# Performance work log

Measured on AMD Instinct MI355X. Metric: run time of the kernel, lower is better.

## Reference

```python
import jax, jax.numpy as jnp
import numpy as np

T, D_MODEL, D_FF, N_EXPERTS, TOP_K = 8192, 1024, 4096, 8, 2

def setup_inputs() -> dict:
    key = jax.random.key(0)
    k1, k2, k3, k4, k5 = jax.random.split(key, 5)
    hidden_states = jax.random.normal(k1, (T, D_MODEL), dtype=jnp.float32)
    # router picks TOP_K distinct-ish experts per token; build one-hot mask [T, K, E]
    expert_idx = jax.random.randint(k2, (T, TOP_K), 0, N_EXPERTS)
    selected_experts = jax.nn.one_hot(expert_idx, N_EXPERTS, dtype=jnp.int32)
    rw = jax.random.uniform(k3, (T, TOP_K), dtype=jnp.float32)
    routing_weights = rw / jnp.sum(rw, axis=-1, keepdims=True)
    scale = 1.0 / np.sqrt(D_MODEL)
    wi = jax.random.normal(k4, (N_EXPERTS, D_FF, D_MODEL), dtype=jnp.float32) * scale
    wo = jax.random.normal(k5, (N_EXPERTS, D_MODEL, D_FF), dtype=jnp.float32) * (1.0 / np.sqrt(D_FF))
    return {"hidden_states": hidden_states, "selected_experts": selected_experts,
            "routing_weights": routing_weights, "wi": wi, "wo": wo}

def reference(hidden_states, selected_experts, routing_weights, wi, wo):
    # expert_mask: [E, K, T] (as in torch permute(2,1,0))
    mask = jnp.transpose(selected_experts, (2, 1, 0)).astype(hidden_states.dtype)
    # combined per-token weight for each expert: w[t, e] = sum_k mask[e,k,t]*routing_weights[t,k]
    w = jnp.einsum('ekt,tk->te', mask, routing_weights)
    out = jnp.zeros_like(hidden_states)
    # fixed small loop over experts; tokens not routed to expert e get weight 0,
    # so this is mathematically identical to the gather->MLP->scale->scatter-add.
    for e in range(wi.shape[0]):
        h = jax.nn.relu(hidden_states @ wi[e].T)     # [T, d_ff] (dropout is identity at eval)
        y = h @ wo[e].T                              # [T, d_model]
        out = out + w[:, e:e + 1] * y
    return out
```

## Files before the change

kernel.cpp:

```cpp
#include <hip/hip_runtime.h>
#include <hip/hip_bf16.h>


#define T_TOK   8192
#define D_MODEL 1024
#define D_FF    4096
#define NE      8
#define BM      128
#define BK      64
#define MT2     72
#define MT_MAX  (MT2 * 2)
#define ROWS_MAX (MT2 * 256)
#define BUFB    32768
#define LDS_G1  98304

typedef float f32x4 __attribute__((ext_vector_type(4)));
typedef short s16x8 __attribute__((ext_vector_type(8)));
typedef short s16x4 __attribute__((ext_vector_type(4)));
typedef unsigned short u16;

__device__ __forceinline__ u16 f2bf(float x) {
  __hip_bfloat16 h = __float2bfloat16(x);
  return *reinterpret_cast<u16*>(&h);
}

__device__ __forceinline__ s16x8 cvt8(float4 a, float4 b) {
  s16x8 v;
  v[0] = (short)f2bf(a.x); v[1] = (short)f2bf(a.y);
  v[2] = (short)f2bf(a.z); v[3] = (short)f2bf(a.w);
  v[4] = (short)f2bf(b.x); v[5] = (short)f2bf(b.y);
  v[6] = (short)f2bf(b.z); v[7] = (short)f2bf(b.w);
  return v;
}

__device__ __forceinline__ void gload_lds16(const void* g, void* l) {
  __builtin_amdgcn_global_load_lds((const __attribute__((address_space(1))) void*)g,
                                   (__attribute__((address_space(3))) void*)l,
                                   16, 0, 0);
}

__global__ void moe_route(const int* __restrict__ sel, const float* __restrict__ rw,
                          int* __restrict__ cnt, int* __restrict__ tidx,
                          float* __restrict__ tw) {
  int t = blockIdx.x * blockDim.x + threadIdx.x;
  if (t >= T_TOK) return;
  int e0 = 0, e1 = 0;
  #pragma unroll
  for (int e = 0; e < NE; ++e) {
    if (sel[t * 16 + e])     e0 = e;
    if (sel[t * 16 + 8 + e]) e1 = e;
  }
  float w0 = rw[2 * t], w1 = rw[2 * t + 1];
  if (e0 == e1) {
    int p = atomicAdd(&cnt[e0], 1);
    tidx[e0 * T_TOK + p] = t; tw[e0 * T_TOK + p] = w0 + w1;
  } else {
    int p = atomicAdd(&cnt[e0], 1);
    tidx[e0 * T_TOK + p] = t; tw[e0 * T_TOK + p] = w0;
    int q = atomicAdd(&cnt[e1], 1);
    tidx[e1 * T_TOK + q] = t; tw[e1 * T_TOK + q] = w1;
  }
}

__global__ void moe_tilemap(const int* __restrict__ cnt, const int* __restrict__ tidx,
                            const float* __restrict__ tw, int* __restrict__ te128,
                            int* __restrict__ te256, int* __restrict__ tokr,
                            float* __restrict__ wr) {
  int off[NE + 1];
  {
    int o = 0;
    #pragma unroll
    for (int e = 0; e < NE; ++e) { off[e] = o; o += (cnt[e] + 255) & ~255; }
    off[NE] = o;
  }
  const int total = off[NE];
  const int gid = blockIdx.x * blockDim.x + threadIdx.x;
  const int stride = gridDim.x * blockDim.x;
  for (int t = gid; t < MT_MAX; t += stride) {
    int r0 = t * 128; int e = -1;
    if (r0 < total) {
      #pragma unroll
      for (int i = NE - 1; i >= 0; --i) if (r0 >= off[i]) { e = i; break; }
    }
    te128[t] = e;
    if ((t & 1) == 0) te256[t >> 1] = e;
  }
  for (int i = gid; i < ROWS_MAX; i += stride) {
    if (i >= total) { tokr[i] = -1; wr[i] = 0.f; continue; }
    int e = 0;
    #pragma unroll
    for (int k = NE - 1; k >= 0; --k) if (i >= off[k]) { e = k; break; }
    int j = i - off[e];
    int ok = j < cnt[e];
    tokr[i] = ok ? tidx[e * T_TOK + j] : -1;
    wr[i]   = ok ? tw[e * T_TOK + j] : 0.f;
  }
}

__global__ void moe_gather_x(const float* __restrict__ hs, const int* __restrict__ tokr,
                             u16* __restrict__ Xg) {
  int row = blockIdx.x;
  int tok = tokr[row];
  int c = threadIdx.x * 4;
  u16* dst = Xg + (size_t)row * D_MODEL + c;
  s16x4 o;
  if (tok < 0) {
    o[0] = o[1] = o[2] = o[3] = 0;
  } else {
    float4 v = *(const float4*)(hs + (size_t)tok * D_MODEL + c);
    o[0] = (short)f2bf(v.x); o[1] = (short)f2bf(v.y);
    o[2] = (short)f2bf(v.z); o[3] = (short)f2bf(v.w);
  }
  *(s16x4*)dst = o;
}

__global__ void moe_cvt_w(const float* __restrict__ wi, const float* __restrict__ wo,
                          u16* __restrict__ wib, u16* __restrict__ wob) {
  const size_t NW = (size_t)NE * D_FF * D_MODEL;
  size_t i = ((size_t)blockIdx.x * blockDim.x + threadIdx.x) * 8;
  const float* src; u16* dst;
  if (i < NW) { src = wi + i; dst = wib + i; }
  else        { src = wo + (i - NW); dst = wob + (i - NW); }
  float4 a = *(const float4*)(src);
  float4 b = *(const float4*)(src + 4);
  *(s16x8*)dst = cvt8(a, b);
}

__global__ void moe_cvt_wi_s(const float* __restrict__ wi, u16* __restrict__ wis,
                             int W, int f0) {
  size_t i = ((size_t)blockIdx.x * blockDim.x + threadIdx.x) * 8;
  size_t per = (size_t)W * D_MODEL;
  int e = (int)(i / per); size_t r = i % per;
  const float* src = wi + ((size_t)e * D_FF + f0) * D_MODEL + r;
  float4 a = *(const float4*)src;
  float4 b = *(const float4*)(src + 4);
  *(s16x8*)(wis + i) = cvt8(a, b);
}

__global__ void moe_cvt_wo_s(const float* __restrict__ wo, u16* __restrict__ wos,
                             int W, int f0) {
  size_t i = ((size_t)blockIdx.x * blockDim.x + threadIdx.x) * 8;
  size_t per = (size_t)D_MODEL * W;
  int e = (int)(i / per); size_t r = i % per;
  int row = (int)(r / W), col = (int)(r % W);
  const float* src = wo + ((size_t)e * D_MODEL + row) * D_FF + f0 + col;
  float4 a = *(const float4*)src;
  float4 b = *(const float4*)(src + 4);
  *(s16x8*)(wos + i) = cvt8(a, b);
}

template <bool FULL>
__global__ __launch_bounds__(512, 1)
void moe_g1(const u16* __restrict__ Xg, const u16* __restrict__ wiP,
            const int* __restrict__ te256, u16* __restrict__ H,
            int W, int f0) {
  extern __shared__ char lds[];
  const int GR = gridDim.x;
  const int task = (blockIdx.x & 7) * (GR >> 3) + (blockIdx.x >> 3);
  const int mt = task % MT2;
  const int nc = task / MT2;
  const int e = te256[mt];
  if (e < 0) return;
  const int grow0 = mt * 256;
  const int fcol = nc * 256;

  const int tid = threadIdx.x;
  const int lane = tid & 63, wv = tid >> 6;
  const int lg = lane >> 4, ll = lane & 15;
  const int wm = wv >> 2, wn = wv & 3;

  const int sw = (tid * 16) ^ (((tid >> 3) & 7) << 4);
  const int srow = sw >> 6, scol = sw & 63;
  const int inner = (ll * 64 + lg * 16) ^ (((ll >> 1) & 7) << 4);

  const char* gA = (const char*)(Xg + (size_t)grow0 * D_MODEL);
  const char* gB = (const char*)(wiP + (FULL ? ((size_t)e * D_FF + f0 + fcol)
                                             : ((size_t)e * W + fcol)) * D_MODEL);

  f32x4 acc[8][4];
  #pragma unroll
  for (int m = 0; m < 8; ++m)
    #pragma unroll
    for (int n = 0; n < 4; ++n) acc[m][n] = (f32x4){0.f, 0.f, 0.f, 0.f};

  auto stage = [&](int kb, char* lbuf) {
    #pragma unroll
    for (int j = 0; j < 2; ++j)
      gload_lds16(gA + (size_t)(j * 128 + srow) * 2048 + kb + scol,
                  lbuf + j * 8192 + tid * 16);
    #pragma unroll
    for (int j = 0; j < 2; ++j)
      gload_lds16(gB + (size_t)(j * 128 + srow) * 2048 + kb + scol,
                  lbuf + 16384 + j * 8192 + tid * 16);
  };

  const int NT = D_MODEL / 32;
  stage(0, lds);
  stage(64, lds + BUFB);
  int bufi = 0;
  for (int t = 0; t < NT; ++t) {
    if (t < NT - 1) { asm volatile("s_waitcnt vmcnt(4)" ::: "memory"); }
    else            { asm volatile("s_waitcnt vmcnt(0)" ::: "memory"); }
    asm volatile("s_barrier" ::: "memory");
    const char* la = lds + bufi * BUFB + wm * 8192;
    const char* lb = lds + bufi * BUFB + 16384 + wn * 4096;
    if (t + 2 < NT) {
      int b2 = bufi + 2; if (b2 >= 3) b2 -= 3;
      stage((t + 2) * 64, lds + b2 * BUFB);
    }
    s16x8 bq0 = *(const s16x8*)(lb + 0 * 1024 + inner);
    s16x8 bq1 = *(const s16x8*)(lb + 1 * 1024 + inner);
    s16x8 bq2 = *(const s16x8*)(lb + 2 * 1024 + inner);
    s16x8 bq3 = *(const s16x8*)(lb + 3 * 1024 + inner);
    {
      s16x8 a0 = *(const s16x8*)(la + 0 * 1024 + inner);
      s16x8 a1 = *(const s16x8*)(la + 1 * 1024 + inner);
      s16x8 a2 = *(const s16x8*)(la + 2 * 1024 + inner);
      s16x8 a3 = *(const s16x8*)(la + 3 * 1024 + inner);
      __builtin_amdgcn_s_setprio(1);
      acc[0][0] = __builtin_amdgcn_mfma_f32_16x16x32_bf16(a0, bq0, acc[0][0], 0, 0, 0);
      acc[0][1] = __builtin_amdgcn_mfma_f32_16x16x32_bf16(a0, bq1, acc[0][1], 0, 0, 0);
      acc[0][2] = __builtin_amdgcn_mfma_f32_16x16x32_bf16(a0, bq2, acc[0][2], 0, 0, 0);
      acc[0][3] = __builtin_amdgcn_mfma_f32_16x16x32_bf16(a0, bq3, acc[0][3], 0, 0, 0);
      acc[1][0] = __builtin_amdgcn_mfma_f32_16x16x32_bf16(a1, bq0, acc[1][0], 0, 0, 0);
      acc[1][1] = __builtin_amdgcn_mfma_f32_16x16x32_bf16(a1, bq1, acc[1][1], 0, 0, 0);
      acc[1][2] = __builtin_amdgcn_mfma_f32_16x16x32_bf16(a1, bq2, acc[1][2], 0, 0, 0);
      acc[1][3] = __builtin_amdgcn_mfma_f32_16x16x32_bf16(a1, bq3, acc[1][3], 0, 0, 0);
      acc[2][0] = __builtin_amdgcn_mfma_f32_16x16x32_bf16(a2, bq0, acc[2][0], 0, 0, 0);
      acc[2][1] = __builtin_amdgcn_mfma_f32_16x16x32_bf16(a2, bq1, acc[2][1], 0, 0, 0);
      acc[2][2] = __builtin_amdgcn_mfma_f32_16x16x32_bf16(a2, bq2, acc[2][2], 0, 0, 0);
      acc[2][3] = __builtin_amdgcn_mfma_f32_16x16x32_bf16(a2, bq3, acc[2][3], 0, 0, 0);
      acc[3][0] = __builtin_amdgcn_mfma_f32_16x16x32_bf16(a3, bq0, acc[3][0], 0, 0, 0);
      acc[3][1] = __builtin_amdgcn_mfma_f32_16x16x32_bf16(a3, bq1, acc[3][1], 0, 0, 0);
      acc[3][2] = __builtin_amdgcn_mfma_f32_16x16x32_bf16(a3, bq2, acc[3][2], 0, 0, 0);
      acc[3][3] = __builtin_amdgcn_mfma_f32_16x16x32_bf16(a3, bq3, acc[3][3], 0, 0, 0);
      __builtin_amdgcn_s_setprio(0);
    }
    __builtin_amdgcn_s_barrier();
    {
      s16x8 a0 = *(const s16x8*)(la + 4 * 1024 + inner);
      s16x8 a1 = *(const s16x8*)(la + 5 * 1024 + inner);
      s16x8 a2 = *(const s16x8*)(la + 6 * 1024 + inner);
      s16x8 a3 = *(const s16x8*)(la + 7 * 1024 + inner);
      __builtin_amdgcn_s_setprio(1);
      acc[4][0] = __builtin_amdgcn_mfma_f32_16x16x32_bf16(a0, bq0, acc[4][0], 0, 0, 0);
      acc[4][1] = __builtin_amdgcn_mfma_f32_16x16x32_bf16(a0, bq1, acc[4][1], 0, 0, 0);
      acc[4][2] = __builtin_amdgcn_mfma_f32_16x16x32_bf16(a0, bq2, acc[4][2], 0, 0, 0);
      acc[4][3] = __builtin_amdgcn_mfma_f32_16x16x32_bf16(a0, bq3, acc[4][3], 0, 0, 0);
      acc[5][0] = __builtin_amdgcn_mfma_f32_16x16x32_bf16(a1, bq0, acc[5][0], 0, 0, 0);
      acc[5][1] = __builtin_amdgcn_mfma_f32_16x16x32_bf16(a1, bq1, acc[5][1], 0, 0, 0);
      acc[5][2] = __builtin_amdgcn_mfma_f32_16x16x32_bf16(a1, bq2, acc[5][2], 0, 0, 0);
      acc[5][3] = __builtin_amdgcn_mfma_f32_16x16x32_bf16(a1, bq3, acc[5][3], 0, 0, 0);
      acc[6][0] = __builtin_amdgcn_mfma_f32_16x16x32_bf16(a2, bq0, acc[6][0], 0, 0, 0);
      acc[6][1] = __builtin_amdgcn_mfma_f32_16x16x32_bf16(a2, bq1, acc[6][1], 0, 0, 0);
      acc[6][2] = __builtin_amdgcn_mfma_f32_16x16x32_bf16(a2, bq2, acc[6][2], 0, 0, 0);
      acc[6][3] = __builtin_amdgcn_mfma_f32_16x16x32_bf16(a2, bq3, acc[6][3], 0, 0, 0);
      acc[7][0] = __builtin_amdgcn_mfma_f32_16x16x32_bf16(a3, bq0, acc[7][0], 0, 0, 0);
      acc[7][1] = __builtin_amdgcn_mfma_f32_16x16x32_bf16(a3, bq1, acc[7][1], 0, 0, 0);
      acc[7][2] = __builtin_amdgcn_mfma_f32_16x16x32_bf16(a3, bq2, acc[7][2], 0, 0, 0);
      acc[7][3] = __builtin_amdgcn_mfma_f32_16x16x32_bf16(a3, bq3, acc[7][3], 0, 0, 0);
      __builtin_amdgcn_s_setprio(0);
    }
    bufi += 1; if (bufi >= 3) bufi -= 3;
  }

  #pragma unroll
  for (int mf = 0; mf < 8; ++mf) {
    #pragma unroll
    for (int r = 0; r < 4; ++r) {
      int row = grow0 + wm * 128 + mf * 16 + lg * 4 + r;
      u16* hp = H + (size_t)row * W + fcol + wn * 64 + ll;
      #pragma unroll
      for (int nf = 0; nf < 4; ++nf) {
        float v = acc[mf][nf][r];
        hp[nf * 16] = f2bf(v > 0.f ? v : 0.f);
      }
    }
  }
}

template <bool FULL>
__global__ __launch_bounds__(256, 4)
void moe_g2(const u16* __restrict__ H, const u16* __restrict__ woP,
            const int* __restrict__ te128, const int* __restrict__ tokr,
            const float* __restrict__ wr, float* __restrict__ out,
            int W, int f0, int KCH) {
  __shared__ u16 As[BM * BK];
  __shared__ u16 Bs[BM * BK];
  __shared__ int s_tok[BM];
  __shared__ float s_w[BM];

  const int GR = gridDim.x;
  const int task = (blockIdx.x & 7) * (GR >> 3) + (blockIdx.x >> 3);
  const int dc = task & 7;
  const int rest = task >> 3;
  const int mt = rest % MT_MAX;
  const int kc = rest / MT_MAX;
  const int e = te128[mt];
  if (e < 0) return;
  const int grow0 = mt * 128;
  const int dcol0 = dc * 128;

  const int tid = threadIdx.x;
  const int lane = tid & 63, wv = tid >> 6;
  const int lg = lane >> 4, ll = lane & 15;
  const int wm = wv >> 1, wn = wv & 1;

  if (tid < BM) { s_tok[tid] = tokr[grow0 + tid]; s_w[tid] = wr[grow0 + tid]; }
  __syncthreads();

  const u16* abase0 = H + (size_t)grow0 * W + (size_t)kc * KCH;
  const size_t bpitch = FULL ? (size_t)D_FF : (size_t)W;
  const u16* bbase0 = woP + ((size_t)e * D_MODEL + dcol0) * bpitch
                      + (FULL ? f0 : 0) + (size_t)kc * KCH;

  f32x4 acc[4][4];
  #pragma unroll
  for (int m = 0; m < 4; ++m)
    #pragma unroll
    for (int n = 0; n < 4; ++n) acc[m][n] = (f32x4){0.f, 0.f, 0.f, 0.f};

  for (int kk = 0; kk < KCH / BK; ++kk) {
    __syncthreads();
    const u16* ab = abase0 + kk * BK;
    #pragma unroll
    for (int i = 0; i < 4; ++i) {
      int off = wv * 4096 + i * 1024 + lane * 16;
      int row = off >> 7, colb = off & 127;
      gload_lds16(ab + (size_t)row * W + (colb >> 1), (char*)As + off);
    }
    const u16* bb = bbase0 + kk * BK;
    #pragma unroll
    for (int i = 0; i < 4; ++i) {
      int off = wv * 4096 + i * 1024 + lane * 16;
      int row = off >> 7, colb = off & 127;
      gload_lds16(bb + (size_t)row * bpitch + (colb >> 1), (char*)Bs + off);
    }
    __syncthreads();
    #pragma unroll
    for (int kb = 0; kb < 2; ++kb) {
      s16x8 af[4], bf[4];
      #pragma unroll
      for (int m = 0; m < 4; ++m)
        af[m] = *(const s16x8*)(As + (wm * 64 + m * 16 + ll) * BK + kb * 32 + lg * 8);
      #pragma unroll
      for (int n = 0; n < 4; ++n)
        bf[n] = *(const s16x8*)(Bs + (wn * 64 + n * 16 + ll) * BK + kb * 32 + lg * 8);
      #pragma unroll
      for (int m = 0; m < 4; ++m)
        #pragma unroll
        for (int n = 0; n < 4; ++n)
          acc[m][n] = __builtin_amdgcn_mfma_f32_16x16x32_bf16(af[m], bf[n], acc[m][n], 0, 0, 0);
    }
  }

  #pragma unroll
  for (int m = 0; m < 4; ++m) {
    #pragma unroll
    for (int r = 0; r < 4; ++r) {
      int row = wm * 64 + m * 16 + lg * 4 + r;
      int tok = s_tok[row];
      if (tok >= 0) {
        float w = s_w[row];
        float* op = out + (size_t)tok * D_MODEL + dcol0 + wn * 64 + ll;
        #pragma unroll
        for (int n = 0; n < 4; ++n)
          atomicAdd(op + n * 16, acc[m][n][r] * w);
      }
    }
  }
}

extern "C" void kernel_launch(void* const* d_in, const int* in_sizes, int n_in,
                              void* d_out, int out_size, void* d_ws, size_t ws_size,
                              hipStream_t stream) {
  const float* hs  = (const float*)d_in[0];
  const int*   sel = (const int*)d_in[1];
  const float* rw  = (const float*)d_in[2];
  const float* wi  = (const float*)d_in[3];
  const float* wo  = (const float*)d_in[4];
  float* out = (float*)d_out;

  const size_t NW   = (size_t)NE * D_FF * D_MODEL;
  const size_t CTRL = 1u << 20;
  const size_t WB   = 2 * NW * sizeof(u16);
  const size_t XGB  = (size_t)ROWS_MAX * D_MODEL * 2;

  bool FULLW = true; int W = D_FF;
  {
    bool found = false;
    for (int f : {1, 2, 4, 8, 16}) {
      int Wc = D_FF / f;
      size_t need = CTRL + WB + XGB + (size_t)ROWS_MAX * Wc * 2;
      if (need <= ws_size) { FULLW = true; W = Wc; found = true; break; }
    }
    if (!found) {
      for (int Wc : {1024, 512, 256}) {
        size_t sl = (size_t)2 * NE * Wc * D_MODEL * 2;
        size_t need = CTRL + sl + XGB + (size_t)ROWS_MAX * Wc * 2;
        if (need <= ws_size) { FULLW = false; W = Wc; break; }
      }
    }
  }
  const int FS = D_FF / W;

  size_t off = 0;
  auto take = [&](size_t b) -> char* {
    char* r = (char*)d_ws + off; off = (off + b + 255) & ~(size_t)255; return r;
  };
  int*   tidx = (int*)take((size_t)NE * T_TOK * 4);
  float* tw   = (float*)take((size_t)NE * T_TOK * 4);
  int*   tokr = (int*)take((size_t)ROWS_MAX * 4);
  float* wrr  = (float*)take((size_t)ROWS_MAX * 4);
  int*   te   = (int*)take(MT_MAX * 4);
  int*   te2  = (int*)take(MT2 * 4);
  int*   cnt  = (int*)take(256);
  off = CTRL;
  u16 *wiP, *woP;
  if (FULLW) { wiP = (u16*)take(NW * 2); woP = (u16*)take(NW * 2); }
  else       { wiP = (u16*)take((size_t)NE * W * D_MODEL * 2);
               woP = (u16*)take((size_t)NE * D_MODEL * W * 2); }
  u16* Xg   = (u16*)take(XGB);
  u16* Hbuf = (u16*)take((size_t)ROWS_MAX * W * 2);

  hipMemsetAsync(cnt, 0, 256, stream);
  hipMemsetAsync(d_out, 0, (size_t)out_size * sizeof(float), stream);
  moe_route<<<T_TOK / 256, 256, 0, stream>>>(sel, rw, cnt, tidx, tw);
  moe_tilemap<<<64, 256, 0, stream>>>(cnt, tidx, tw, te, te2, tokr, wrr);
  moe_gather_x<<<ROWS_MAX, 256, 0, stream>>>(hs, tokr, Xg);
  if (FULLW)
    moe_cvt_w<<<(int)(2 * NW / 8 / 256), 256, 0, stream>>>(wi, wo, wiP, woP);

  hipFuncSetAttribute(reinterpret_cast<const void*>(&moe_g1<true>),
                      hipFuncAttributeMaxDynamicSharedMemorySize, LDS_G1);
  hipFuncSetAttribute(reinterpret_cast<const void*>(&moe_g1<false>),
                      hipFuncAttributeMaxDynamicSharedMemorySize, LDS_G1);

  const int KCH = (W >= 2048) ? 2048 : W;
  const int g1grid = MT2 * (W / 256);
  const int g2grid = MT_MAX * 8 * (W / KCH);
  const int cvtblk = (int)(((size_t)NE * W * D_MODEL / 8) / 256);

  for (int p = 0; p < FS; ++p) {
    const int f0 = p * W;
    if (!FULLW) {
      moe_cvt_wi_s<<<cvtblk, 256, 0, stream>>>(wi, wiP, W, f0);
      moe_cvt_wo_s<<<cvtblk, 256, 0, stream>>>(wo, woP, W, f0);
    }
    if (FULLW) {
      moe_g1<true><<<g1grid, 512, LDS_G1, stream>>>(Xg, wiP, te2, Hbuf, W, f0);
      moe_g2<true><<<g2grid, 256, 0, stream>>>(Hbuf, woP, te, tokr, wrr, out, W, f0, KCH);
    } else {
      moe_g1<false><<<g1grid, 512, LDS_G1, stream>>>(Xg, wiP, te2, Hbuf, W, f0);
      moe_g2<false><<<g2grid, 256, 0, stream>>>(Hbuf, woP, te, tokr, wrr, out, W, f0, KCH);
    }
  }
}
```

Measured before the change: 549.0 us.

## Port second expert GEMM to 256x256 triple-buffered LDS pipeline shared with first GEMM

The down-projection GEMM now uses the same 256x256-tile, 512-thread, triple-buffered async-LDS pipeline as the up-projection. It previously used a 128x128, single-buffered tile. The pipeline body is factored into a macro with configurable pitches. The split-K chunk shrinks from 2048 to 1024, so there are more K-splits and more atomic adds to the output. The goal is better MFMA utilization and data reuse, at the cost of lower occupancy and extra atomic traffic.

```diff
diff --git a/kernel.cpp b/kernel.cpp
--- a/kernel.cpp
+++ b/kernel.cpp
@@ -6,8 +6,6 @@
 #define D_MODEL 1024
 #define D_FF    4096
 #define NE      8
-#define BM      128
-#define BK      64
 #define MT2     72
 #define MT_MAX  (MT2 * 2)
 #define ROWS_MAX (MT2 * 256)
@@ -63,9 +61,8 @@
 }
 
 __global__ void moe_tilemap(const int* __restrict__ cnt, const int* __restrict__ tidx,
-                            const float* __restrict__ tw, int* __restrict__ te128,
-                            int* __restrict__ te256, int* __restrict__ tokr,
-                            float* __restrict__ wr) {
+                            const float* __restrict__ tw, int* __restrict__ te256,
+                            int* __restrict__ tokr, float* __restrict__ wr) {
   int off[NE + 1];
   {
     int o = 0;
@@ -76,14 +73,13 @@
   const int total = off[NE];
   const int gid = blockIdx.x * blockDim.x + threadIdx.x;
   const int stride = gridDim.x * blockDim.x;
-  for (int t = gid; t < MT_MAX; t += stride) {
-    int r0 = t * 128; int e = -1;
+  for (int t = gid; t < MT2; t += stride) {
+    int r0 = t * 256; int e = -1;
     if (r0 < total) {
       #pragma unroll
       for (int i = NE - 1; i >= 0; --i) if (r0 >= off[i]) { e = i; break; }
     }
-    te128[t] = e;
-    if ((t & 1) == 0) te256[t >> 1] = e;
+    te256[t] = e;
   }
   for (int i = gid; i < ROWS_MAX; i += stride) {
     if (i >= total) { tokr[i] = -1; wr[i] = 0.f; continue; }
@@ -148,6 +144,86 @@
   float4 b = *(const float4*)(src + 4);
   *(s16x8*)(wos + i) = cvt8(a, b);
 }
+
+#define K_PIPE_BODY(NT_, PITCH_A, PITCH_B)                                        \
+  auto stage = [&](int kb, char* lbuf) {                                          \
+    _Pragma("unroll")                                                             \
+    for (int j = 0; j < 2; ++j)                                                   \
+      gload_lds16(gA + (size_t)(j * 128 + srow) * (PITCH_A) + kb + scol,          \
+                  lbuf + j * 8192 + tid * 16);                                    \
+    _Pragma("unroll")                                                             \
+    for (int j = 0; j < 2; ++j)                                                   \
+      gload_lds16(gB + (size_t)(j * 128 + srow) * (PITCH_B) + kb + scol,          \
+                  lbuf + 16384 + j * 8192 + tid * 16);                            \
+  };                                                                              \
+  stage(0, lds);                                                                  \
+  stage(64, lds + BUFB);                                                          \
+  int bufi = 0;                                                                   \
+  for (int t = 0; t < (NT_); ++t) {                                               \
+    if (t < (NT_) - 1) { asm volatile("s_waitcnt vmcnt(4)" ::: "memory"); }       \
+    else               { asm volatile("s_waitcnt vmcnt(0)" ::: "memory"); }       \
+    asm volatile("s_barrier" ::: "memory");                                       \
+    const char* la = lds + bufi * BUFB + wm * 8192;                               \
+    const char* lb = lds + bufi * BUFB + 16384 + wn * 4096;                       \
+    if (t + 2 < (NT_)) {                                                          \
+      int b2 = bufi + 2; if (b2 >= 3) b2 -= 3;                                    \
+      stage((t + 2) * 64, lds + b2 * BUFB);                                       \
+    }                                                                             \
+    s16x8 bq0 = *(const s16x8*)(lb + 0 * 1024 + inner);                           \
+    s16x8 bq1 = *(const s16x8*)(lb + 1 * 1024 + inner);                           \
+    s16x8 bq2 = *(const s16x8*)(lb + 2 * 1024 + inner);                           \
+    s16x8 bq3 = *(const s16x8*)(lb + 3 * 1024 + inner);                           \
+    {                                                                             \
+      s16x8 a0 = *(const s16x8*)(la + 0 * 1024 + inner);                          \
+      s16x8 a1 = *(const s16x8*)(la + 1 * 1024 + inner);                          \
+      s16x8 a2 = *(const s16x8*)(la + 2 * 1024 + inner);                          \
+      s16x8 a3 = *(const s16x8*)(la + 3 * 1024 + inner);                          \
+      __builtin_amdgcn_s_setprio(1);                                              \
+      acc[0][0] = __builtin_amdgcn_mfma_f32_16x16x32_bf16(a0, bq0, acc[0][0], 0, 0, 0); \
+      acc[0][1] = __builtin_amdgcn_mfma_f32_16x16x32_bf16(a0, bq1, acc[0][1], 0, 0, 0); \
+      acc[0][2] = __builtin_amdgcn_mfma_f32_16x16x32_bf16(a0, bq2, acc[0][2], 0, 0, 0); \
+      acc[0][3] = __builtin_amdgcn_mfma_f32_16x16x32_bf16(a0, bq3, acc[0][3], 0, 0, 0); \
+      acc[1][0] = __builtin_amdgcn_mfma_f32_16x16x32_bf16(a1, bq0, acc[1][0], 0, 0, 0); \
+      acc[1][1] = __builtin_amdgcn_mfma_f32_16x16x32_bf16(a1, bq1, acc[1][1], 0, 0, 0); \
+      acc[1][2] = __builtin_amdgcn_mfma_f32_16x16x32_bf16(a1, bq2, acc[1][2], 0, 0, 0); \
+      acc[1][3] = __builtin_amdgcn_mfma_f32_16x16x32_bf16(a1, bq3, acc[1][3], 0, 0, 0); \
+      acc[2][0] = __builtin_amdgcn_mfma_f32_16x16x32_bf16(a2, bq0, acc[2][0], 0, 0, 0); \
+      acc[2][1] = __builtin_amdgcn_mfma_f32_16x16x32_bf16(a2, bq1, acc[2][1], 0, 0, 0); \
+      acc[2][2] = __builtin_amdgcn_mfma_f32_16x16x32_bf16(a2, bq2, acc[2][2], 0, 0, 0); \
+      acc[2][3] = __builtin_amdgcn_mfma_f32_16x16x32_bf16(a2, bq3, acc[2][3], 0, 0, 0); \
+      acc[3][0] = __builtin_amdgcn_mfma_f32_16x16x32_bf16(a3, bq0, acc[3][0], 0, 0, 0); \
+      acc[3][1] = __builtin_amdgcn_mfma_f32_16x16x32_bf16(a3, bq1, acc[3][1], 0, 0, 0); \
+      acc[3][2] = __builtin_amdgcn_mfma_f32_16x16x32_bf16(a3, bq2, acc[3][2], 0, 0, 0); \
+      acc[3][3] = __builtin_amdgcn_mfma_f32_16x16x32_bf16(a3, bq3, acc[3][3], 0, 0, 0); \
+      __builtin_amdgcn_s_setprio(0);                                              \
+    }                                                                             \
+    __builtin_amdgcn_s_barrier();                                                 \
+    {                                                                             \
+      s16x8 a0 = *(const s16x8*)(la + 4 * 1024 + inner);                          \
+      s16x8 a1 = *(const s16x8*)(la + 5 * 1024 + inner);                          \
+      s16x8 a2 = *(const s16x8*)(la + 6 * 1024 + inner);                          \
+      s16x8 a3 = *(const s16x8*)(la + 7 * 1024 + inner);                          \
+      __builtin_amdgcn_s_setprio(1);                                              \
+      acc[4][0] = __builtin_amdgcn_mfma_f32_16x16x32_bf16(a0, bq0, acc[4][0], 0, 0, 0); \
+      acc[4][1] = __builtin_amdgcn_mfma_f32_16x16x32_bf16(a0, bq1, acc[4][1], 0, 0, 0); \
+      acc[4][2] = __builtin_amdgcn_mfma_f32_16x16x32_bf16(a0, bq2, acc[4][2], 0, 0, 0); \
+      acc[4][3] = __builtin_amdgcn_mfma_f32_16x16x32_bf16(a0, bq3, acc[4][3], 0, 0, 0); \
+      acc[5][0] = __builtin_amdgcn_mfma_f32_16x16x32_bf16(a1, bq0, acc[5][0], 0, 0, 0); \
+      acc[5][1] = __builtin_amdgcn_mfma_f32_16x16x32_bf16(a1, bq1, acc[5][1], 0, 0, 0); \
+      acc[5][2] = __builtin_amdgcn_mfma_f32_16x16x32_bf16(a1, bq2, acc[5][2], 0, 0, 0); \
+      acc[5][3] = __builtin_amdgcn_mfma_f32_16x16x32_bf16(a1, bq3, acc[5][3], 0, 0, 0); \
+      acc[6][0] = __builtin_amdgcn_mfma_f32_16x16x32_bf16(a2, bq0, acc[6][0], 0, 0, 0); \
+      acc[6][1] = __builtin_amdgcn_mfma_f32_16x16x32_bf16(a2, bq1, acc[6][1], 0, 0, 0); \
+      acc[6][2] = __builtin_amdgcn_mfma_f32_16x16x32_bf16(a2, bq2, acc[6][2], 0, 0, 0); \
+      acc[6][3] = __builtin_amdgcn_mfma_f32_16x16x32_bf16(a2, bq3, acc[6][3], 0, 0, 0); \
+      acc[7][0] = __builtin_amdgcn_mfma_f32_16x16x32_bf16(a3, bq0, acc[7][0], 0, 0, 0); \
+      acc[7][1] = __builtin_amdgcn_mfma_f32_16x16x32_bf16(a3, bq1, acc[7][1], 0, 0, 0); \
+      acc[7][2] = __builtin_amdgcn_mfma_f32_16x16x32_bf16(a3, bq2, acc[7][2], 0, 0, 0); \
+      acc[7][3] = __builtin_amdgcn_mfma_f32_16x16x32_bf16(a3, bq3, acc[7][3], 0, 0, 0); \
+      __builtin_amdgcn_s_setprio(0);                                              \
+    }                                                                             \
+    bufi += 1; if (bufi >= 3) bufi -= 3;                                          \
+  }
 
 template <bool FULL>
 __global__ __launch_bounds__(512, 1)
@@ -183,86 +259,8 @@
     #pragma unroll
     for (int n = 0; n < 4; ++n) acc[m][n] = (f32x4){0.f, 0.f, 0.f, 0.f};
 
-  auto stage = [&](int kb, char* lbuf) {
-    #pragma unroll
-    for (int j = 0; j < 2; ++j)
-      gload_lds16(gA + (size_t)(j * 128 + srow) * 2048 + kb + scol,
-                  lbuf + j * 8192 + tid * 16);
-    #pragma unroll
-    for (int j = 0; j < 2; ++j)
-      gload_lds16(gB + (size_t)(j * 128 + srow) * 2048 + kb + scol,
-                  lbuf + 16384 + j * 8192 + tid * 16);
-  };
-
   const int NT = D_MODEL / 32;
-  stage(0, lds);
-  stage(64, lds + BUFB);
-  int bufi = 0;
-  for (int t = 0; t < NT; ++t) {
-    if (t < NT - 1) { asm volatile("s_waitcnt vmcnt(4)" ::: "memory"); }
-    else            { asm volatile("s_waitcnt vmcnt(0)" ::: "memory"); }
-    asm volatile("s_barrier" ::: "memory");
-    const char* la = lds + bufi * BUFB + wm * 8192;
-    const char* lb = lds + bufi * BUFB + 16384 + wn * 4096;
-    if (t + 2 < NT) {
-      int b2 = bufi + 2; if (b2 >= 3) b2 -= 3;
-      stage((t + 2) * 64, lds + b2 * BUFB);
-    }
-    s16x8 bq0 = *(const s16x8*)(lb + 0 * 1024 + inner);
-    s16x8 bq1 = *(const s16x8*)(lb + 1 * 1024 + inner);
-    s16x8 bq2 = *(const s16x8*)(lb + 2 * 1024 + inner);
-    s16x8 bq3 = *(const s16x8*)(lb + 3 * 1024 + inner);
-    {
-      s16x8 a0 = *(const s16x8*)(la + 0 * 1024 + inner);
-      s16x8 a1 = *(const s16x8*)(la + 1 * 1024 + inner);
-      s16x8 a2 = *(const s16x8*)(la + 2 * 1024 + inner);
-      s16x8 a3 = *(const s16x8*)(la + 3 * 1024 + inner);
-      __builtin_amdgcn_s_setprio(1);
-      acc[0][0] = __builtin_amdgcn_mfma_f32_16x16x32_bf16(a0, bq0, acc[0][0], 0, 0, 0);
-      acc[0][1] = __builtin_amdgcn_mfma_f32_16x16x32_bf16(a0, bq1, acc[0][1], 0, 0, 0);
-      acc[0][2] = __builtin_amdgcn_mfma_f32_16x16x32_bf16(a0, bq2, acc[0][2], 0, 0, 0);
-      acc[0][3] = __builtin_amdgcn_mfma_f32_16x16x32_bf16(a0, bq3, acc[0][3], 0, 0, 0);
-      acc[1][0] = __builtin_amdgcn_mfma_f32_16x16x32_bf16(a1, bq0, acc[1][0], 0, 0, 0);
-      acc[1][1] = __builtin_amdgcn_mfma_f32_16x16x32_bf16(a1, bq1, acc[1][1], 0, 0, 0);
-      acc[1][2] = __builtin_amdgcn_mfma_f32_16x16x32_bf16(a1, bq2, acc[1][2], 0, 0, 0);
-      acc[1][3] = __builtin_amdgcn_mfma_f32_16x16x32_bf16(a1, bq3, acc[1][3], 0, 0, 0);
-      acc[2][0] = __builtin_amdgcn_mfma_f32_16x16x32_bf16(a2, bq0, acc[2][0], 0, 0, 0);
-      acc[2][1] = __builtin_amdgcn_mfma_f32_16x16x32_bf16(a2, bq1, acc[2][1], 0, 0, 0);
-      acc[2][2] = __builtin_amdgcn_mfma_f32_16x16x32_bf16(a2, bq2, acc[2][2], 0, 0, 0);
-      acc[2][3] = __builtin_amdgcn_mfma_f32_16x16x32_bf16(a2, bq3, acc[2][3], 0, 0, 0);
-      acc[3][0] = __builtin_amdgcn_mfma_f32_16x16x32_bf16(a3, bq0, acc[3][0], 0, 0, 0);
-      acc[3][1] = __builtin_amdgcn_mfma_f32_16x16x32_bf16(a3, bq1, acc[3][1], 0, 0, 0);
-      acc[3][2] = __builtin_amdgcn_mfma_f32_16x16x32_bf16(a3, bq2, acc[3][2], 0, 0, 0);
-      acc[3][3] = __builtin_amdgcn_mfma_f32_16x16x32_bf16(a3, bq3, acc[3][3], 0, 0, 0);
-      __builtin_amdgcn_s_setprio(0);
-    }
-    __builtin_amdgcn_s_barrier();
-    {
-      s16x8 a0 = *(const s16x8*)(la + 4 * 1024 + inner);
-      s16x8 a1 = *(const s16x8*)(la + 5 * 1024 + inner);
-      s16x8 a2 = *(const s16x8*)(la + 6 * 1024 + inner);
-      s16x8 a3 = *(const s16x8*)(la + 7 * 1024 + inner);
-      __builtin_amdgcn_s_setprio(1);
-      acc[4][0] = __builtin_amdgcn_mfma_f32_16x16x32_bf16(a0, bq0, acc[4][0], 0, 0, 0);
-      acc[4][1] = __builtin_amdgcn_mfma_f32_16x16x32_bf16(a0, bq1, acc[4][1], 0, 0, 0);
-      acc[4][2] = __builtin_amdgcn_mfma_f32_16x16x32_bf16(a0, bq2, acc[4][2], 0, 0, 0);
-      acc[4][3] = __builtin_amdgcn_mfma_f32_16x16x32_bf16(a0, bq3, acc[4][3], 0, 0, 0);
-      acc[5][0] = __builtin_amdgcn_mfma_f32_16x16x32_bf16(a1, bq0, acc[5][0], 0, 0, 0);
-      acc[5][1] = __builtin_amdgcn_mfma_f32_16x16x32_bf16(a1, bq1, acc[5][1], 0, 0, 0);
-      acc[5][2] = __builtin_amdgcn_mfma_f32_16x16x32_bf16(a1, bq2, acc[5][2], 0, 0, 0);
-      acc[5][3] = __builtin_amdgcn_mfma_f32_16x16x32_bf16(a1, bq3, acc[5][3], 0, 0, 0);
-      acc[6][0] = __builtin_amdgcn_mfma_f32_16x16x32_bf16(a2, bq0, acc[6][0], 0, 0, 0);
-      acc[6][1] = __builtin_amdgcn_mfma_f32_16x16x32_bf16(a2, bq1, acc[6][1], 0, 0, 0);
-      acc[6][2] = __builtin_amdgcn_mfma_f32_16x16x32_bf16(a2, bq2, acc[6][2], 0, 0, 0);
-      acc[6][3] = __builtin_amdgcn_mfma_f32_16x16x32_bf16(a2, bq3, acc[6][3], 0, 0, 0);
-      acc[7][0] = __builtin_amdgcn_mfma_f32_16x16x32_bf16(a3, bq0, acc[7][0], 0, 0, 0);
-      acc[7][1] = __builtin_amdgcn_mfma_f32_16x16x32_bf16(a3, bq1, acc[7][1], 0, 0, 0);
-      acc[7][2] = __builtin_amdgcn_mfma_f32_16x16x32_bf16(a3, bq2, acc[7][2], 0, 0, 0);
-      acc[7][3] = __builtin_amdgcn_mfma_f32_16x16x32_bf16(a3, bq3, acc[7][3], 0, 0, 0);
-      __builtin_amdgcn_s_setprio(0);
-    }
-    bufi += 1; if (bufi >= 3) bufi -= 3;
-  }
+  K_PIPE_BODY(NT, 2048, 2048)
 
   #pragma unroll
   for (int mf = 0; mf < 8; ++mf) {
@@ -280,92 +278,59 @@
 }
 
 template <bool FULL>
-__global__ __launch_bounds__(256, 4)
+__global__ __launch_bounds__(512, 1)
 void moe_g2(const u16* __restrict__ H, const u16* __restrict__ woP,
-            const int* __restrict__ te128, const int* __restrict__ tokr,
+            const int* __restrict__ te256, const int* __restrict__ tokr,
             const float* __restrict__ wr, float* __restrict__ out,
             int W, int f0, int KCH) {
-  __shared__ u16 As[BM * BK];
-  __shared__ u16 Bs[BM * BK];
-  __shared__ int s_tok[BM];
-  __shared__ float s_w[BM];
-
+  extern __shared__ char lds[];
   const int GR = gridDim.x;
   const int task = (blockIdx.x & 7) * (GR >> 3) + (blockIdx.x >> 3);
-  const int dc = task & 7;
-  const int rest = task >> 3;
-  const int mt = rest % MT_MAX;
-  const int kc = rest / MT_MAX;
-  const int e = te128[mt];
+  const int dc = task & 3;
+  const int rest = task >> 2;
+  const int mt = rest % MT2;
+  const int kc = rest / MT2;
+  const int e = te256[mt];
   if (e < 0) return;
-  const int grow0 = mt * 128;
-  const int dcol0 = dc * 128;
+  const int grow0 = mt * 256;
+  const int dcol0 = dc * 256;
 
   const int tid = threadIdx.x;
   const int lane = tid & 63, wv = tid >> 6;
   const int lg = lane >> 4, ll = lane & 15;
-  const int wm = wv >> 1, wn = wv & 1;
-
-  if (tid < BM) { s_tok[tid] = tokr[grow0 + tid]; s_w[tid] = wr[grow0 + tid]; }
-  __syncthreads();
-
-  const u16* abase0 = H + (size_t)grow0 * W + (size_t)kc * KCH;
-  const size_t bpitch = FULL ? (size_t)D_FF : (size_t)W;
-  const u16* bbase0 = woP + ((size_t)e * D_MODEL + dcol0) * bpitch
-                      + (FULL ? f0 : 0) + (size_t)kc * KCH;
-
-  f32x4 acc[4][4];
+  const int wm = wv >> 2, wn = wv & 3;
+
+  const int sw = (tid * 16) ^ (((tid >> 3) & 7) << 4);
+  const int srow = sw >> 6, scol = sw & 63;
+  const int inner = (ll * 64 + lg * 16) ^ (((ll >> 1) & 7) << 4);
+
+  const size_t pA = (size_t)W * 2;
+  const size_t pB = (FULL ? (size_t)D_FF : (size_t)W) * 2;
+  const char* gA = (const char*)(H + (size_t)grow0 * W + (size_t)kc * KCH);
+  const char* gB = (const char*)(woP + ((size_t)e * D_MODEL + dcol0) * (pB / 2)
+                                 + (FULL ? f0 : 0) + (size_t)kc * KCH);
+
+  f32x4 acc[8][4];
   #pragma unroll
-  for (int m = 0; m < 4; ++m)
+  for (int m = 0; m < 8; ++m)
     #pragma unroll
     for (int n = 0; n < 4; ++n) acc[m][n] = (f32x4){0.f, 0.f, 0.f, 0.f};
 
-  for (int kk = 0; kk < KCH / BK; ++kk) {
-    __syncthreads();
-    const u16* ab = abase0 + kk * BK;
-    #pragma unroll
-    for (int i = 0; i < 4; ++i) {
-      int off = wv * 4096 + i * 1024 + lane * 16;
-      int row = off >> 7, colb = off & 127;
-      gload_lds16(ab + (size_t)row * W + (colb >> 1), (char*)As + off);
-    }
-    const u16* bb = bbase0 + kk * BK;
-    #pragma unroll
-    for (int i = 0; i < 4; ++i) {
-      int off = wv * 4096 + i * 1024 + lane * 16;
-      int row = off >> 7, colb = off & 127;
-      gload_lds16(bb + (size_t)row * bpitch + (colb >> 1), (char*)Bs + off);
-    }
-    __syncthreads();
-    #pragma unroll
-    for (int kb = 0; kb < 2; ++kb) {
-      s16x8 af[4], bf[4];
-      #pragma unroll
-      for (int m = 0; m < 4; ++m)
-        af[m] = *(const s16x8*)(As + (wm * 64 + m * 16 + ll) * BK + kb * 32 + lg * 8);
-      #pragma unroll
-      for (int n = 0; n < 4; ++n)
-        bf[n] = *(const s16x8*)(Bs + (wn * 64 + n * 16 + ll) * BK + kb * 32 + lg * 8);
-      #pragma unroll
-      for (int m = 0; m < 4; ++m)
-        #pragma unroll
-        for (int n = 0; n < 4; ++n)
-          acc[m][n] = __builtin_amdgcn_mfma_f32_16x16x32_bf16(af[m], bf[n], acc[m][n], 0, 0, 0);
-    }
-  }
+  const int NT = KCH / 32;
+  K_PIPE_BODY(NT, pA, pB)
 
   #pragma unroll
-  for (int m = 0; m < 4; ++m) {
+  for (int mf = 0; mf < 8; ++mf) {
     #pragma unroll
     for (int r = 0; r < 4; ++r) {
-      int row = wm * 64 + m * 16 + lg * 4 + r;
-      int tok = s_tok[row];
+      int row = grow0 + wm * 128 + mf * 16 + lg * 4 + r;
+      int tok = tokr[row];
       if (tok >= 0) {
-        float w = s_w[row];
+        float w = wr[row];
         float* op = out + (size_t)tok * D_MODEL + dcol0 + wn * 64 + ll;
         #pragma unroll
-        for (int n = 0; n < 4; ++n)
-          atomicAdd(op + n * 16, acc[m][n][r] * w);
+        for (int nf = 0; nf < 4; ++nf)
+          atomicAdd(op + nf * 16, acc[mf][nf][r] * w);
       }
     }
   }
@@ -412,7 +377,6 @@
   float* tw   = (float*)take((size_t)NE * T_TOK * 4);
   int*   tokr = (int*)take((size_t)ROWS_MAX * 4);
   float* wrr  = (float*)take((size_t)ROWS_MAX * 4);
-  int*   te   = (int*)take(MT_MAX * 4);
   int*   te2  = (int*)take(MT2 * 4);
   int*   cnt  = (int*)take(256);
   off = CTRL;
@@ -426,7 +390,7 @@
   hipMemsetAsync(cnt, 0, 256, stream);
   hipMemsetAsync(d_out, 0, (size_t)out_size * sizeof(float), stream);
   moe_route<<<T_TOK / 256, 256, 0, stream>>>(sel, rw, cnt, tidx, tw);
-  moe_tilemap<<<64, 256, 0, stream>>>(cnt, tidx, tw, te, te2, tokr, wrr);
+  moe_tilemap<<<64, 256, 0, stream>>>(cnt, tidx, tw, te2, tokr, wrr);
   moe_gather_x<<<ROWS_MAX, 256, 0, stream>>>(hs, tokr, Xg);
   if (FULLW)
     moe_cvt_w<<<(int)(2 * NW / 8 / 256), 256, 0, stream>>>(wi, wo, wiP, woP);
@@ -435,10 +399,14 @@
                       hipFuncAttributeMaxDynamicSharedMemorySize, LDS_G1);
   hipFuncSetAttribute(reinterpret_cast<const void*>(&moe_g1<false>),
                       hipFuncAttributeMaxDynamicSharedMemorySize, LDS_G1);
-
-  const int KCH = (W >= 2048) ? 2048 : W;
+  hipFuncSetAttribute(reinterpret_cast<const void*>(&moe_g2<true>),
+                      hipFuncAttributeMaxDynamicSharedMemorySize, LDS_G1);
+  hipFuncSetAttribute(reinterpret_cast<const void*>(&moe_g2<false>),
+                      hipFuncAttributeMaxDynamicSharedMemorySize, LDS_G1);
+
+  const int KCH = (W >= 1024) ? 1024 : W;
   const int g1grid = MT2 * (W / 256);
-  const int g2grid = MT_MAX * 8 * (W / KCH);
+  const int g2grid = MT2 * 4 * (W / KCH);
   const int cvtblk = (int)(((size_t)NE * W * D_MODEL / 8) / 256);
 
   for (int p = 0; p < FS; ++p) {
@@ -449,10 +417,12 @@
     }
     if (FULLW) {
       moe_g1<true><<<g1grid, 512, LDS_G1, stream>>>(Xg, wiP, te2, Hbuf, W, f0);
-      moe_g2<true><<<g2grid, 256, 0, stream>>>(Hbuf, woP, te, tokr, wrr, out, W, f0, KCH);
+      moe_g2<true><<<g2grid, 512, LDS_G1, stream>>>(Hbuf, woP, te2, tokr, wrr,
+                                                    out, W, f0, KCH);
     } else {
       moe_g1<false><<<g1grid, 512, LDS_G1, stream>>>(Xg, wiP, te2, Hbuf, W, f0);
-      moe_g2<false><<<g2grid, 256, 0, stream>>>(Hbuf, woP, te, tokr, wrr, out, W, f0, KCH);
-    }
-  }
-}
+      moe_g2<false><<<g2grid, 512, LDS_G1, stream>>>(Hbuf, woP, te2, tokr, wrr,
+                                                     out, W, f0, KCH);
+    }
+  }
+}
```

Measured after the change: 663.3 us. +20.8%, slower.

## Rewrite second expert GEMM with 256-row tiles and triple-buffered LDS pipeline

Applied to the files above, without the earlier changes.

The down-projection kernel moves from 128-row tiles with 256 threads and single-buffered static LDS to 256-row tiles with 512 threads, a three-stage dynamic-LDS ring with swizzled layout, and explicit vmcnt waits with raw barriers. Loads for step t+2 are issued while MFMAs run on step t, and setprio is raised around the MFMA block. The aim is to hide global load latency and cut LDS bank conflicts. The split-K factor is fixed at 2, and the tokr/wr lookups in the epilogue now read global memory instead of shared memory. The cost is more LDS per block, which may lower occupancy.

```diff
diff --git a/kernel.cpp b/kernel.cpp
--- a/kernel.cpp
+++ b/kernel.cpp
@@ -6,13 +6,12 @@
 #define D_MODEL 1024
 #define D_FF    4096
 #define NE      8
-#define BM      128
-#define BK      64
 #define MT2     72
-#define MT_MAX  (MT2 * 2)
 #define ROWS_MAX (MT2 * 256)
 #define BUFB    32768
 #define LDS_G1  98304
+#define BUF2    24576
+#define LDS_G2  73728
 
 typedef float f32x4 __attribute__((ext_vector_type(4)));
 typedef short s16x8 __attribute__((ext_vector_type(8)));
@@ -63,9 +62,8 @@
 }
 
 __global__ void moe_tilemap(const int* __restrict__ cnt, const int* __restrict__ tidx,
-                            const float* __restrict__ tw, int* __restrict__ te128,
-                            int* __restrict__ te256, int* __restrict__ tokr,
-                            float* __restrict__ wr) {
+                            const float* __restrict__ tw, int* __restrict__ te256,
+                            int* __restrict__ tokr, float* __restrict__ wr) {
   int off[NE + 1];
   {
     int o = 0;
@@ -76,14 +74,13 @@
   const int total = off[NE];
   const int gid = blockIdx.x * blockDim.x + threadIdx.x;
   const int stride = gridDim.x * blockDim.x;
-  for (int t = gid; t < MT_MAX; t += stride) {
-    int r0 = t * 128; int e = -1;
+  for (int t = gid; t < MT2; t += stride) {
+    int r0 = t * 256; int e = -1;
     if (r0 < total) {
       #pragma unroll
       for (int i = NE - 1; i >= 0; --i) if (r0 >= off[i]) { e = i; break; }
     }
-    te128[t] = e;
-    if ((t & 1) == 0) te256[t >> 1] = e;
+    te256[t] = e;
   }
   for (int i = gid; i < ROWS_MAX; i += stride) {
     if (i >= total) { tokr[i] = -1; wr[i] = 0.f; continue; }
@@ -280,25 +277,21 @@
 }
 
 template <bool FULL>
-__global__ __launch_bounds__(256, 4)
+__global__ __launch_bounds__(512, 4)
 void moe_g2(const u16* __restrict__ H, const u16* __restrict__ woP,
-            const int* __restrict__ te128, const int* __restrict__ tokr,
+            const int* __restrict__ te256, const int* __restrict__ tokr,
             const float* __restrict__ wr, float* __restrict__ out,
             int W, int f0, int KCH) {
-  __shared__ u16 As[BM * BK];
-  __shared__ u16 Bs[BM * BK];
-  __shared__ int s_tok[BM];
-  __shared__ float s_w[BM];
-
+  extern __shared__ char lds[];
   const int GR = gridDim.x;
   const int task = (blockIdx.x & 7) * (GR >> 3) + (blockIdx.x >> 3);
   const int dc = task & 7;
   const int rest = task >> 3;
-  const int mt = rest % MT_MAX;
-  const int kc = rest / MT_MAX;
-  const int e = te128[mt];
+  const int mt = rest % MT2;
+  const int kc = rest / MT2;
+  const int e = te256[mt];
   if (e < 0) return;
-  const int grow0 = mt * 128;
+  const int grow0 = mt * 256;
   const int dcol0 = dc * 128;
 
   const int tid = threadIdx.x;
@@ -306,13 +299,15 @@
   const int lg = lane >> 4, ll = lane & 15;
   const int wm = wv >> 1, wn = wv & 1;
 
-  if (tid < BM) { s_tok[tid] = tokr[grow0 + tid]; s_w[tid] = wr[grow0 + tid]; }
-  __syncthreads();
-
-  const u16* abase0 = H + (size_t)grow0 * W + (size_t)kc * KCH;
-  const size_t bpitch = FULL ? (size_t)D_FF : (size_t)W;
-  const u16* bbase0 = woP + ((size_t)e * D_MODEL + dcol0) * bpitch
-                      + (FULL ? f0 : 0) + (size_t)kc * KCH;
+  const int sw = (tid * 16) ^ (((tid >> 3) & 7) << 4);
+  const int srow = sw >> 6, scol = sw & 63;
+  const int inner = (ll * 64 + lg * 16) ^ (((ll >> 1) & 7) << 4);
+
+  const size_t pA = (size_t)W * 2;
+  const size_t pB = (FULL ? (size_t)D_FF : (size_t)W) * 2;
+  const char* gA = (const char*)(H + (size_t)grow0 * W) + (size_t)kc * KCH * 2;
+  const char* gB = (const char*)(woP + ((size_t)e * D_MODEL + dcol0) * (pB / 2)
+                                 + (FULL ? f0 : 0)) + (size_t)kc * KCH * 2;
 
   f32x4 acc[4][4];
   #pragma unroll
@@ -320,52 +315,73 @@
     #pragma unroll
     for (int n = 0; n < 4; ++n) acc[m][n] = (f32x4){0.f, 0.f, 0.f, 0.f};
 
-  for (int kk = 0; kk < KCH / BK; ++kk) {
-    __syncthreads();
-    const u16* ab = abase0 + kk * BK;
-    #pragma unroll
-    for (int i = 0; i < 4; ++i) {
-      int off = wv * 4096 + i * 1024 + lane * 16;
-      int row = off >> 7, colb = off & 127;
-      gload_lds16(ab + (size_t)row * W + (colb >> 1), (char*)As + off);
-    }
-    const u16* bb = bbase0 + kk * BK;
-    #pragma unroll
-    for (int i = 0; i < 4; ++i) {
-      int off = wv * 4096 + i * 1024 + lane * 16;
-      int row = off >> 7, colb = off & 127;
-      gload_lds16(bb + (size_t)row * bpitch + (colb >> 1), (char*)Bs + off);
-    }
-    __syncthreads();
-    #pragma unroll
-    for (int kb = 0; kb < 2; ++kb) {
-      s16x8 af[4], bf[4];
-      #pragma unroll
-      for (int m = 0; m < 4; ++m)
-        af[m] = *(const s16x8*)(As + (wm * 64 + m * 16 + ll) * BK + kb * 32 + lg * 8);
-      #pragma unroll
-      for (int n = 0; n < 4; ++n)
-        bf[n] = *(const s16x8*)(Bs + (wn * 64 + n * 16 + ll) * BK + kb * 32 + lg * 8);
-      #pragma unroll
-      for (int m = 0; m < 4; ++m)
-        #pragma unroll
-        for (int n = 0; n < 4; ++n)
-          acc[m][n] = __builtin_amdgcn_mfma_f32_16x16x32_bf16(af[m], bf[n], acc[m][n], 0, 0, 0);
-    }
+  auto stage = [&](int kb, char* lbuf) {
+    #pragma unroll
+    for (int j = 0; j < 2; ++j)
+      gload_lds16(gA + (size_t)(j * 128 + srow) * pA + kb + scol,
+                  lbuf + j * 8192 + tid * 16);
+    {
+      int brow = srow & 127;
+      gload_lds16(gB + (size_t)brow * pB + kb + ((sw & 8191) & 63)
+                  , lbuf + 16384 + (tid & 511) * 16);
+    }
+  };
+
+  const int NT = KCH / 32;
+  stage(0, lds);
+  stage(64, lds + BUF2);
+  int bufi = 0;
+  for (int t = 0; t < NT; ++t) {
+    if (t < NT - 1) { asm volatile("s_waitcnt vmcnt(3)" ::: "memory"); }
+    else            { asm volatile("s_waitcnt vmcnt(0)" ::: "memory"); }
+    asm volatile("s_barrier" ::: "memory");
+    const char* la = lds + bufi * BUF2 + wm * 4096;
+    const char* lb = lds + bufi * BUF2 + 16384 + wn * 4096;
+    if (t + 2 < NT) {
+      int b2 = bufi + 2; if (b2 >= 3) b2 -= 3;
+      stage((t + 2) * 64, lds + b2 * BUF2);
+    }
+    s16x8 bq0 = *(const s16x8*)(lb + 0 * 1024 + inner);
+    s16x8 bq1 = *(const s16x8*)(lb + 1 * 1024 + inner);
+    s16x8 bq2 = *(const s16x8*)(lb + 2 * 1024 + inner);
+    s16x8 bq3 = *(const s16x8*)(lb + 3 * 1024 + inner);
+    s16x8 a0 = *(const s16x8*)(la + 0 * 1024 + inner);
+    s16x8 a1 = *(const s16x8*)(la + 1 * 1024 + inner);
+    s16x8 a2 = *(const s16x8*)(la + 2 * 1024 + inner);
+    s16x8 a3 = *(const s16x8*)(la + 3 * 1024 + inner);
+    __builtin_amdgcn_s_setprio(1);
+    acc[0][0] = __builtin_amdgcn_mfma_f32_16x16x32_bf16(a0, bq0, acc[0][0], 0, 0, 0);
+    acc[0][1] = __builtin_amdgcn_mfma_f32_16x16x32_bf16(a0, bq1, acc[0][1], 0, 0, 0);
+    acc[0][2] = __builtin_amdgcn_mfma_f32_16x16x32_bf16(a0, bq2, acc[0][2], 0, 0, 0);
+    acc[0][3] = __builtin_amdgcn_mfma_f32_16x16x32_bf16(a0, bq3, acc[0][3], 0, 0, 0);
+    acc[1][0] = __builtin_amdgcn_mfma_f32_16x16x32_bf16(a1, bq0, acc[1][0], 0, 0, 0);
+    acc[1][1] = __builtin_amdgcn_mfma_f32_16x16x32_bf16(a1, bq1, acc[1][1], 0, 0, 0);
+    acc[1][2] = __builtin_amdgcn_mfma_f32_16x16x32_bf16(a1, bq2, acc[1][2], 0, 0, 0);
+    acc[1][3] = __builtin_amdgcn_mfma_f32_16x16x32_bf16(a1, bq3, acc[1][3], 0, 0, 0);
+    acc[2][0] = __builtin_amdgcn_mfma_f32_16x16x32_bf16(a2, bq0, acc[2][0], 0, 0, 0);
+    acc[2][1] = __builtin_amdgcn_mfma_f32_16x16x32_bf16(a2, bq1, acc[2][1], 0, 0, 0);
+    acc[2][2] = __builtin_amdgcn_mfma_f32_16x16x32_bf16(a2, bq2, acc[2][2], 0, 0, 0);
+    acc[2][3] = __builtin_amdgcn_mfma_f32_16x16x32_bf16(a2, bq3, acc[2][3], 0, 0, 0);
+    acc[3][0] = __builtin_amdgcn_mfma_f32_16x16x32_bf16(a3, bq0, acc[3][0], 0, 0, 0);
+    acc[3][1] = __builtin_amdgcn_mfma_f32_16x16x32_bf16(a3, bq1, acc[3][1], 0, 0, 0);
+    acc[3][2] = __builtin_amdgcn_mfma_f32_16x16x32_bf16(a3, bq2, acc[3][2], 0, 0, 0);
+    acc[3][3] = __builtin_amdgcn_mfma_f32_16x16x32_bf16(a3, bq3, acc[3][3], 0, 0, 0);
+    __builtin_amdgcn_s_setprio(0);
+    bufi += 1; if (bufi >= 3) bufi -= 3;
   }
 
   #pragma unroll
-  for (int m = 0; m < 4; ++m) {
+  for (int mf = 0; mf < 4; ++mf) {
     #pragma unroll
     for (int r = 0; r < 4; ++r) {
-      int row = wm * 64 + m * 16 + lg * 4 + r;
-      int tok = s_tok[row];
+      int row = grow0 + wm * 64 + mf * 16 + lg * 4 + r;
+      int tok = tokr[row];
       if (tok >= 0) {
-        float w = s_w[row];
+        float w = wr[row];
         float* op = out + (size_t)tok * D_MODEL + dcol0 + wn * 64 + ll;
         #pragma unroll
-        for (int n = 0; n < 4; ++n)
-          atomicAdd(op + n * 16, acc[m][n][r] * w);
+        for (int nf = 0; nf < 4; ++nf)
+          atomicAdd(op + nf * 16, acc[mf][nf][r] * w);
       }
     }
   }
@@ -412,7 +428,6 @@
   float* tw   = (float*)take((size_t)NE * T_TOK * 4);
   int*   tokr = (int*)take((size_t)ROWS_MAX * 4);
   float* wrr  = (float*)take((size_t)ROWS_MAX * 4);
-  int*   te   = (int*)take(MT_MAX * 4);
   int*   te2  = (int*)take(MT2 * 4);
   int*   cnt  = (int*)take(256);
   off = CTRL;
@@ -426,7 +441,7 @@
   hipMemsetAsync(cnt, 0, 256, stream);
   hipMemsetAsync(d_out, 0, (size_t)out_size * sizeof(float), stream);
   moe_route<<<T_TOK / 256, 256, 0, stream>>>(sel, rw, cnt, tidx, tw);
-  moe_tilemap<<<64, 256, 0, stream>>>(cnt, tidx, tw, te, te2, tokr, wrr);
+  moe_tilemap<<<64, 256, 0, stream>>>(cnt, tidx, tw, te2, tokr, wrr);
   moe_gather_x<<<ROWS_MAX, 256, 0, stream>>>(hs, tokr, Xg);
   if (FULLW)
     moe_cvt_w<<<(int)(2 * NW / 8 / 256), 256, 0, stream>>>(wi, wo, wiP, woP);
@@ -435,10 +450,14 @@
                       hipFuncAttributeMaxDynamicSharedMemorySize, LDS_G1);
   hipFuncSetAttribute(reinterpret_cast<const void*>(&moe_g1<false>),
                       hipFuncAttributeMaxDynamicSharedMemorySize, LDS_G1);
-
-  const int KCH = (W >= 2048) ? 2048 : W;
+  hipFuncSetAttribute(reinterpret_cast<const void*>(&moe_g2<true>),
+                      hipFuncAttributeMaxDynamicSharedMemorySize, LDS_G2);
+  hipFuncSetAttribute(reinterpret_cast<const void*>(&moe_g2<false>),
+                      hipFuncAttributeMaxDynamicSharedMemorySize, LDS_G2);
+
+  const int KCH = W / 2;
   const int g1grid = MT2 * (W / 256);
-  const int g2grid = MT_MAX * 8 * (W / KCH);
+  const int g2grid = MT2 * 8 * 2;
   const int cvtblk = (int)(((size_t)NE * W * D_MODEL / 8) / 256);
 
   for (int p = 0; p < FS; ++p) {
@@ -449,10 +468,12 @@
     }
     if (FULLW) {
       moe_g1<true><<<g1grid, 512, LDS_G1, stream>>>(Xg, wiP, te2, Hbuf, W, f0);
-      moe_g2<true><<<g2grid, 256, 0, stream>>>(Hbuf, woP, te, tokr, wrr, out, W, f0, KCH);
+      moe_g2<true><<<g2grid, 512, LDS_G2, stream>>>(Hbuf, woP, te2, tokr, wrr,
+                                                    out, W, f0, KCH);
     } else {
       moe_g1<false><<<g1grid, 512, LDS_G1, stream>>>(Xg, wiP, te2, Hbuf, W, f0);
-      moe_g2<false><<<g2grid, 256, 0, stream>>>(Hbuf, woP, te, tokr, wrr, out, W, f0, KCH);
-    }
-  }
-}
+      moe_g2<false><<<g2grid, 512, LDS_G2, stream>>>(Hbuf, woP, te2, tokr, wrr,
+                                                     out, W, f0, KCH);
+    }
+  }
+}
```

Result: faster. 537.1 us (-2.2%).
